# Optimization experiments

Measured on AMD Instinct MI355X. Metric: run time of the kernel, lower is better.

The kernel has to match this reference:

```python
import jax, jax.numpy as jnp
import numpy as np
from jax import lax
import math

B, L, D = 2, 1024, 1024
H = 16
HD = D // H
DS = 16            # d_state
EXP = 2
DIN = EXP * D      # d_inner = 2048
DCONV = 4
DTR = math.ceil(D / 16)  # dt_rank = 64
EPS = 1e-5


def setup_inputs() -> dict:
    key = jax.random.key(0)
    ks = jax.random.split(key, 24)
    g = lambda i, shape, s=0.02: (jax.random.normal(ks[i], shape, dtype=jnp.float32) * s)
    A_log = jnp.log(jnp.tile(jnp.arange(1, DS + 1, dtype=jnp.float32)[None, :], (DIN, 1)))
    return {
        "x": jax.random.normal(ks[0], (B, L, D), dtype=jnp.float32),
        # MambaWrapper pre-norm
        "mnorm_w": jnp.ones((D,), jnp.float32), "mnorm_b": jnp.zeros((D,), jnp.float32),
        # MambaBlock params
        "in_proj_w": g(1, (2 * DIN, D)),
        "conv_w": g(2, (DIN, 1, DCONV), 0.1), "conv_b": jnp.zeros((DIN,), jnp.float32),
        "x_proj_w": g(3, (DTR + 2 * DS, DIN)),
        "dt_proj_w": g(4, (DIN, DTR)), "dt_proj_b": g(5, (DIN,), 0.01),
        "A_log": A_log, "D_skip": jnp.ones((DIN,), jnp.float32),
        "out_proj_w": g(6, (D, DIN)),
        # attention branch
        "norm1_w": jnp.ones((D,), jnp.float32), "norm1_b": jnp.zeros((D,), jnp.float32),
        "wqkv_w": g(7, (D + 2 * HD, D)), "wqkv_b": jnp.zeros((D + 2 * HD,), jnp.float32),
        "oattn_w": g(8, (D, D)), "oattn_b": jnp.zeros((D,), jnp.float32),
        # parallel fusion: Linear(2D->D) + LayerNorm
        "fuse_w": g(9, (D, 2 * D)), "fuse_b": jnp.zeros((D,), jnp.float32),
        "fln_w": jnp.ones((D,), jnp.float32), "fln_b": jnp.zeros((D,), jnp.float32),
    }


def _ln(x, w, b):
    m = x.mean(-1, keepdims=True)
    xc = x - m
    v = (xc * xc).mean(-1, keepdims=True)
    return xc * lax.rsqrt(v + EPS) * w + b


def _selective_scan(u, delta, A, Bm, Cm, D_skip):
    # u, delta: (b,l,din); A: (din,n); Bm,Cm: (b,l,n)
    dA = jnp.exp(delta[..., None] * A)                    # (b,l,din,n)
    dBu = delta[..., None] * Bm[:, :, None, :] * u[..., None]

    def step(h, inp):
        dA_t, dBu_t, C_t = inp                            # (b,din,n),(b,din,n),(b,n)
        h = dA_t * h + dBu_t
        y = jnp.einsum('bdn,bn->bd', h, C_t)
        return h, y

    h0 = jnp.zeros((u.shape[0], u.shape[2], A.shape[1]), u.dtype)
    _, ys = lax.scan(step, h0, (dA.transpose(1, 0, 2, 3), dBu.transpose(1, 0, 2, 3), Cm.transpose(1, 0, 2)))
    return ys.transpose(1, 0, 2) + u * D_skip             # (b,l,din)


def _mamba_branch(x, mnorm_w, mnorm_b, in_proj_w, conv_w, conv_b, x_proj_w,
                  dt_proj_w, dt_proj_b, A_log, D_skip, out_proj_w):
    xn = _ln(x, mnorm_w, mnorm_b)
    xr = xn @ in_proj_w.T                                 # (b,l,2*din)
    u, res = xr[..., :DIN], xr[..., DIN:]
    # depthwise causal conv1d (torch pads d_conv-1 both sides then slices [:l])
    uc = u.transpose(0, 2, 1)                             # (b,din,l)
    uc = lax.conv_general_dilated(uc, conv_w, (1,), [(DCONV - 1, 0)],
                                  dimension_numbers=('NCH', 'OIH', 'NCH'),
                                  feature_group_count=DIN) + conv_b[None, :, None]
    u = jax.nn.silu(uc.transpose(0, 2, 1))
    dbc = u @ x_proj_w.T                                  # (b,l,dtr+2n)
    delta = jax.nn.softplus(dbc[..., :DTR] @ dt_proj_w.T + dt_proj_b)
    Bm = dbc[..., DTR:DTR + DS]
    Cm = dbc[..., DTR + DS:]
    y = _selective_scan(u, delta, -jnp.exp(A_log), Bm, Cm, D_skip)
    y = y * jax.nn.silu(res)
    return (y @ out_proj_w.T) + x                         # dropout=identity (eval), +residual


def _mqa_branch(x, norm1_w, norm1_b, wqkv_w, wqkv_b, oattn_w, oattn_b):
    xn = _ln(x, norm1_w, norm1_b)
    qkv = xn @ wqkv_w.T + wqkv_b
    q = qkv[..., :D].reshape(B, L, H, HD)
    k = qkv[..., D:D + HD]                                # shared single K head (b,l,hd)
    v = qkv[..., D + HD:]
    scores = jnp.einsum('blhd,bsd->bhls', q, k) / math.sqrt(HD)
    causal = jnp.tril(jnp.ones((L, L), bool))
    scores = jnp.where(causal, scores, jnp.finfo(scores.dtype).min)
    attn = jax.nn.softmax(scores, axis=-1)
    o = jnp.einsum('bhls,bsd->blhd', attn, v).reshape(B, L, D)
    return x + (o @ oattn_w.T + oattn_b)


def reference(x, mnorm_w, mnorm_b, in_proj_w, conv_w, conv_b, x_proj_w,
              dt_proj_w, dt_proj_b, A_log, D_skip, out_proj_w,
              norm1_w, norm1_b, wqkv_w, wqkv_b, oattn_w, oattn_b,
              fuse_w, fuse_b, fln_w, fln_b):
    mamba_out = _mamba_branch(x, mnorm_w, mnorm_b, in_proj_w, conv_w, conv_b, x_proj_w,
                              dt_proj_w, dt_proj_b, A_log, D_skip, out_proj_w)
    attn_out = _mqa_branch(x, norm1_w, norm1_b, wqkv_w, wqkv_b, oattn_w, oattn_b)
    combined = jnp.concatenate([mamba_out, attn_out], axis=-1)
    fused = _ln(combined @ fuse_w.T + fuse_b, fln_w, fln_b)
    return fused
```

## Files before the change

kernel.cpp:

```cpp
#include <hip/hip_runtime.h>
#include <hip/hip_bf16.h>
#include <hip/hip_fp16.h>
#include <cstddef>


using bf16 = __hip_bfloat16;
using frag8 = __attribute__((ext_vector_type(8))) short;
using f32x4 = __attribute__((ext_vector_type(4))) float;

__device__ __forceinline__ float siluf(float x) { return x / (1.f + __expf(-x)); }

__device__ __forceinline__ int sigmode(const unsigned int* sig) {
    const unsigned int s = *sig;
    return s == 0x3F800000u ? 1 : (s == 0x3C003C00u ? 2 : 0);
}
__device__ __forceinline__ float ldx(const void* p, size_t i, int m) {
    if (m == 1) return reinterpret_cast<const float*>(p)[i];
    if (m == 2) return __half2float(reinterpret_cast<const __half*>(p)[i]);
    return __bfloat162float(reinterpret_cast<const bf16*>(p)[i]);
}

__device__ __forceinline__ void gload_lds16(const void* g, void* l) {
    __builtin_amdgcn_global_load_lds(
        (const __attribute__((address_space(1))) unsigned int*)g,
        (__attribute__((address_space(3))) unsigned int*)l, 16, 0, 0);
}

__global__ void sentinel_kernel(float* out, float code) {
    if (threadIdx.x == 0) out[0] = code;
}

__global__ __launch_bounds__(256) void wconv_kernel(const void* __restrict__ W, size_t off,
                                                    bf16* __restrict__ dst, int total8,
                                                    const unsigned int* __restrict__ sig) {
    const int g = blockIdx.x * 256 + threadIdx.x;
    if (g >= total8) return;
    const int md = sigmode(sig);
    const size_t i0 = off + (size_t)g * 8;
    union { bf16 h[8]; uint4 v; } u;
    if (md == 0) {
        u.v = *reinterpret_cast<const uint4*>((const bf16*)W + i0);
    } else {
#pragma unroll
        for (int j = 0; j < 8; ++j) u.h[j] = __float2bfloat16(ldx(W, i0 + j, md));
    }
    *reinterpret_cast<uint4*>(dst + (size_t)g * 8) = u.v;
}

__global__ __launch_bounds__(256) void wconv2_kernel(
    const void* __restrict__ W1, bf16* __restrict__ dst1, int total8_1,
    const void* __restrict__ W2, bf16* __restrict__ dst2, int total8_2,
    const unsigned int* __restrict__ sig) {
    const int g = blockIdx.x * 256 + threadIdx.x;
    const int md = sigmode(sig);
    const void* W;
    bf16* dst;
    int gg;
    if (g < total8_1) { W = W1; dst = dst1; gg = g; }
    else if (g < total8_1 + total8_2) { W = W2; dst = dst2; gg = g - total8_1; }
    else return;
    const size_t i0 = (size_t)gg * 8;
    union { bf16 h[8]; uint4 v; } u;
    if (md == 0) {
        u.v = *reinterpret_cast<const uint4*>((const bf16*)W + i0);
    } else {
#pragma unroll
        for (int j = 0; j < 8; ++j) u.h[j] = __float2bfloat16(ldx(W, i0 + j, md));
    }
    *reinterpret_cast<uint4*>(dst + i0) = u.v;
}

template <typename TO>
__global__ __launch_bounds__(256) void ln_kernel(
    const void* __restrict__ x, int x_from_in,
    const void* __restrict__ w, const void* __restrict__ b,
    const unsigned int* __restrict__ sig, TO* __restrict__ out) {
    const int md = sigmode(sig);
    const int xm = x_from_in ? md : 0;
    const int row = blockIdx.x;
    const int tid = threadIdx.x;
    __shared__ float red[256];
    const size_t base = (size_t)row * 1024;
    float v[4];
    float s = 0.f;
#pragma unroll
    for (int i = 0; i < 4; ++i) { v[i] = ldx(x, base + tid + i * 256, xm); s += v[i]; }
    red[tid] = s;
    __syncthreads();
    for (int st = 128; st > 0; st >>= 1) {
        if (tid < st) red[tid] += red[tid + st];
        __syncthreads();
    }
    const float mean = red[0] * (1.f / 1024.f);
    __syncthreads();
    float s2 = 0.f;
#pragma unroll
    for (int i = 0; i < 4; ++i) { v[i] -= mean; s2 += v[i] * v[i]; }
    red[tid] = s2;
    __syncthreads();
    for (int st = 128; st > 0; st >>= 1) {
        if (tid < st) red[tid] += red[tid + st];
        __syncthreads();
    }
    const float inv = rsqrtf(red[0] * (1.f / 1024.f) + 1e-5f);
#pragma unroll
    for (int i = 0; i < 4; ++i) {
        const int d = tid + i * 256;
        const float r = v[i] * inv * ldx(w, d, md) + ldx(b, d, md);
        if constexpr (sizeof(TO) == 4) out[base + d] = r;
        else out[base + d] = __float2bfloat16(r);
    }
}

template <int BM>
__global__ __launch_bounds__(256) void mfma_gemm(
    const bf16* __restrict__ A1, const bf16* __restrict__ A2, int KA1, int lda,
    const bf16* __restrict__ Wb,
    const void* __restrict__ bias,
    const void* __restrict__ resid, int ldr,
    bf16* __restrict__ C, int ldc,
    int K, int Nbound, int act, const unsigned int* __restrict__ sig,
    bf16* __restrict__ vt) {
    constexpr int NFR = (BM == 128) ? 4 : 2;
    const int md = sigmode(sig);
    __shared__ __align__(16) bf16 Als[BM * 32];
    __shared__ __align__(16) bf16 Wls[128 * 32];
    const int tid = threadIdx.x;
    const int lane = tid & 63;
    const int w = tid >> 6;
    const int arow = (BM == 128) ? ((w >> 1) * 64) : 0;
    const int bcol = (BM == 128) ? ((w & 1) * 64) : (w * 32);
    const int m0 = blockIdx.y * BM;
    const int n0 = blockIdx.x * 128;
    f32x4 acc[4][NFR];
#pragma unroll
    for (int i = 0; i < 4; ++i)
#pragma unroll
        for (int j = 0; j < NFR; ++j) acc[i][j] = {0.f, 0.f, 0.f, 0.f};
    const int fm = lane & 15;
    const int fq = lane >> 4;
    for (int kk = 0; kk < K; kk += 32) {
        if constexpr (BM == 128) {
#pragma unroll
            for (int i = 0; i < 2; ++i) {
                const int chunk = i * 256 + tid;
                const int r = chunk >> 2, q = chunk & 3;
                const int gk = kk + q * 8;
                const bf16* srcA = (A2 != nullptr && gk >= KA1)
                    ? (A2 + (size_t)(m0 + r) * lda + (gk - KA1))
                    : (A1 + (size_t)(m0 + r) * lda + gk);
                gload_lds16(srcA, (char*)Als + (size_t)(i * 256 + w * 64) * 16);
            }
        } else {
            const int r = tid >> 2, q = tid & 3;
            const int gk = kk + q * 8;
            const bf16* srcA = (A2 != nullptr && gk >= KA1)
                ? (A2 + (size_t)(m0 + r) * lda + (gk - KA1))
                : (A1 + (size_t)(m0 + r) * lda + gk);
            gload_lds16(srcA, (char*)Als + (size_t)(w * 64) * 16);
        }
#pragma unroll
        for (int i = 0; i < 2; ++i) {
            const int chunk = i * 256 + tid;
            const int r = chunk >> 2, q = chunk & 3;
            const bf16* srcW = Wb + (size_t)(n0 + r) * K + kk + q * 8;
            gload_lds16(srcW, (char*)Wls + (size_t)(i * 256 + w * 64) * 16);
        }
        __syncthreads();
        frag8 af[4], bfr[NFR];
#pragma unroll
        for (int ms = 0; ms < 4; ++ms)
            af[ms] = *reinterpret_cast<const frag8*>(&Als[(size_t)(arow + ms * 16 + fm) * 32 + fq * 8]);
#pragma unroll
        for (int ns = 0; ns < NFR; ++ns)
            bfr[ns] = *reinterpret_cast<const frag8*>(&Wls[(size_t)(bcol + ns * 16 + fm) * 32 + fq * 8]);
#pragma unroll
        for (int ms = 0; ms < 4; ++ms)
#pragma unroll
            for (int ns = 0; ns < NFR; ++ns)
                acc[ms][ns] = __builtin_amdgcn_mfma_f32_16x16x32_bf16(af[ms], bfr[ns], acc[ms][ns], 0, 0, 0);
        __syncthreads();
    }
#pragma unroll
    for (int ms = 0; ms < 4; ++ms) {
#pragma unroll
        for (int r = 0; r < 4; ++r) {
            const int m = m0 + arow + ms * 16 + fq * 4 + r;
#pragma unroll
            for (int ns = 0; ns < NFR; ++ns) {
                const int n = n0 + bcol + ns * 16 + fm;
                if (n < Nbound) {
                    float v = acc[ms][ns][r];
                    if (bias) v += ldx(bias, n, md);
                    if (resid) v += ldx(resid, (size_t)m * ldr + n, md);
                    if (act == 1) v = (v > 20.f) ? v : log1pf(expf(v));
                    const bf16 hv = __float2bfloat16(v);
                    C[(size_t)m * ldc + n] = hv;
                    if (vt != nullptr && n >= 1088) {
                        vt[((size_t)((m >> 10) * 64 + (n - 1088))) * 1024 + (m & 1023)] = hv;
                    }
                }
            }
        }
    }
}

__global__ __launch_bounds__(256) void conv_silu_kernel(
    const bf16* __restrict__ u0, int us, const void* __restrict__ cw,
    const void* __restrict__ cb, const unsigned int* __restrict__ sig,
    bf16* __restrict__ u) {
    const int md = sigmode(sig);
    const int idx = blockIdx.x * 256 + threadIdx.x;
    const int c8 = (idx & 255) * 8;
    const int bl = idx >> 8;
    const int l = bl & 1023;
    float acc[8];
#pragma unroll
    for (int i = 0; i < 8; ++i) acc[i] = ldx(cb, c8 + i, md);
#pragma unroll
    for (int k = 0; k < 4; ++k) {
        const int ls = l - 3 + k;
        if (ls >= 0) {
            union { frag8 v; bf16 h[8]; } uin;
            uin.v = *reinterpret_cast<const frag8*>(u0 + (size_t)(bl - 3 + k) * us + c8);
#pragma unroll
            for (int i = 0; i < 8; ++i)
                acc[i] += __bfloat162float(uin.h[i]) * ldx(cw, (c8 + i) * 4 + k, md);
        }
    }
    union { frag8 v; bf16 h[8]; } uo;
#pragma unroll
    for (int i = 0; i < 8; ++i) uo.h[i] = __float2bfloat16(siluf(acc[i]));
    *reinterpret_cast<frag8*>(u + (size_t)bl * 2048 + c8) = uo.v;
}

__global__ __launch_bounds__(512) void scan_kernel(
    bf16* __restrict__ delta_y, const bf16* __restrict__ u,
    const bf16* __restrict__ dbc, const bf16* __restrict__ res,
    const void* __restrict__ A_log, const void* __restrict__ D_skip,
    const unsigned int* __restrict__ sig) {
    constexpr int DYS = 4096;
    constexpr int US  = 2048;
    constexpr int BS  = 96;
    constexpr int PRS = 20;
    constexpr int PJS = 168;
    const int md = sigmode(sig);
    const int n = threadIdx.x & 15;
    const int j = threadIdx.x >> 4;
    const int bx = blockIdx.x;
    const int c = ((bx & 7) << 8) | (bx >> 3);
    const int b = blockIdx.y;
    __shared__ float Ac[32 * 17], Hc[32 * 17], h0s[32 * 17];
    __shared__ __align__(16) float P[32 * PJS];
    __shared__ __align__(16) bf16 Dcol[1024], Ucol[1024];
    const float acoef = -expf(ldx(A_log, c * 16 + n, md));
    const float dsk = ldx(D_skip, c, md);
    const int t0 = j * 32;
    const int bt0 = b * 1024 + t0;

    {
        const int tid = threadIdx.x;
#pragma unroll
        for (int rr = 0; rr < 2; ++rr) {
            const int t = tid + rr * 512;
            Dcol[t] = delta_y[(size_t)(b * 1024 + t) * DYS + c];
            Ucol[t] = u[(size_t)(b * 1024 + t) * US + c];
        }
    }
    __syncthreads();

    {
        const bf16* pb = dbc + (size_t)bt0 * BS + 64 + n;
        float hloc = 0.f, aprod = 1.f;
#pragma unroll 8
        for (int tt = 0; tt < 32; ++tt) {
            const float dlt = __bfloat162float(Dcol[t0 + tt]);
            const float ut = __bfloat162float(Ucol[t0 + tt]);
            const float Bn = __bfloat162float(*pb);
            const float a = __expf(dlt * acoef);
            hloc = a * hloc + dlt * Bn * ut;
            aprod *= a;
            pb += BS;
        }
        Ac[j * 17 + n] = aprod;
        Hc[j * 17 + n] = hloc;
    }
    __syncthreads();
    if (threadIdx.x < 16) {
        float e = 0.f;
        for (int jj = 0; jj < 32; ++jj) {
            h0s[jj * 17 + threadIdx.x] = e;
            e = Ac[jj * 17 + threadIdx.x] * e + Hc[jj * 17 + threadIdx.x];
        }
    }
    __syncthreads();

    float h = h0s[j * 17 + n];
    float psum[2];
    float* Pj = &P[j * PJS];
    {
        const bf16* pb = dbc + (size_t)bt0 * BS + 64 + n;
        const int nq = n >> 3;
        const int nr = n & 7;
#pragma unroll
        for (int q = 0; q < 4; ++q) {
#pragma unroll
            for (int k = 0; k < 8; ++k) {
                const int tt = q * 8 + k;
                const float dlt = __bfloat162float(Dcol[t0 + tt]);
                const float ut = __bfloat162float(Ucol[t0 + tt]);
                const float Bn = __bfloat162float(pb[0]);
                const float Cn = __bfloat162float(pb[16]);
                const float a = __expf(dlt * acoef);
                h = a * h + dlt * Bn * ut;
                Pj[k * PRS + n] = h * Cn;
                pb += BS;
            }
            if (nq == (q & 1)) {
                const f32x4* pr = reinterpret_cast<const f32x4*>(&Pj[nr * PRS]);
                float s = 0.f;
#pragma unroll
                for (int v = 0; v < 4; ++v) {
                    const f32x4 q4 = pr[v];
                    s += q4[0] + q4[1] + q4[2] + q4[3];
                }
                psum[q >> 1] = s;
            }
        }
    }
#pragma unroll
    for (int half = 0; half < 2; ++half) {
        const int tl = t0 + half * 16 + n;
        const size_t id = (size_t)(b * 1024 + tl) * DYS + c;
        const float ut = __bfloat162float(Ucol[tl]);
        const float r = __bfloat162float(res[id]);
        delta_y[id] = __float2bfloat16((psum[half] + ut * dsk) * siluf(r));
    }
}

__global__ __launch_bounds__(128) void attn_mfma(const bf16* __restrict__ qkv,
                                                 const bf16* __restrict__ Vt,
                                                 bf16* __restrict__ o) {
    const int tid = threadIdx.x;
    const int lane = tid & 63;
    const int wv = tid >> 6;
    const int fm = lane & 15, quad = lane >> 4;
    const int qt = blockIdx.x, h = blockIdx.y, b = blockIdx.z;
    __shared__ __align__(16) bf16 Pls[2][64][72];
    __shared__ float Ols[64][68];
    __shared__ float Mst[64], Lst[64];

    frag8 qf[4][2];
#pragma unroll
    for (int ms = 0; ms < 4; ++ms)
#pragma unroll
        for (int kq = 0; kq < 2; ++kq)
            qf[ms][kq] = *reinterpret_cast<const frag8*>(
                qkv + ((size_t)(b * 1024 + qt * 64 + ms * 16 + fm)) * 1152 + h * 64 + kq * 32 + quad * 8);

    float mrun[4][4], lrun[4][4];
    f32x4 acco[4][4];
#pragma unroll
    for (int ms = 0; ms < 4; ++ms)
#pragma unroll
        for (int r = 0; r < 4; ++r) { mrun[ms][r] = -1.0e30f; lrun[ms][r] = 0.f; }
#pragma unroll
    for (int ms = 0; ms < 4; ++ms)
#pragma unroll
        for (int nd = 0; nd < 4; ++nd) acco[ms][nd] = {0.f, 0.f, 0.f, 0.f};

    for (int st = wv; st <= qt; st += 2) {
        f32x4 accs[4][4];
#pragma unroll
        for (int ms = 0; ms < 4; ++ms)
#pragma unroll
            for (int ns = 0; ns < 4; ++ns) accs[ms][ns] = {0.f, 0.f, 0.f, 0.f};
        __builtin_amdgcn_s_setprio(1);
#pragma unroll
        for (int ns = 0; ns < 4; ++ns) {
            frag8 kf[2];
#pragma unroll
            for (int kq = 0; kq < 2; ++kq)
                kf[kq] = *reinterpret_cast<const frag8*>(
                    qkv + ((size_t)(b * 1024 + st * 64 + ns * 16 + fm)) * 1152 + 1024 + kq * 32 + quad * 8);
#pragma unroll
            for (int ms = 0; ms < 4; ++ms) {
                accs[ms][ns] = __builtin_amdgcn_mfma_f32_16x16x32_bf16(qf[ms][0], kf[0], accs[ms][ns], 0, 0, 0);
                accs[ms][ns] = __builtin_amdgcn_mfma_f32_16x16x32_bf16(qf[ms][1], kf[1], accs[ms][ns], 0, 0, 0);
            }
        }
        __builtin_amdgcn_s_setprio(0);
        const bool diag = (st == qt);
#pragma unroll
        for (int ms = 0; ms < 4; ++ms) {
            float alpha[4];
#pragma unroll
            for (int r = 0; r < 4; ++r) {
                const int ql = ms * 16 + quad * 4 + r;
                float sv[4];
#pragma unroll
                for (int ns = 0; ns < 4; ++ns) {
                    const int sl = ns * 16 + fm;
                    sv[ns] = (!diag || sl <= ql) ? accs[ms][ns][r] * 0.125f : -1.0e30f;
                }
                float mloc = fmaxf(fmaxf(sv[0], sv[1]), fmaxf(sv[2], sv[3]));
                mloc = fmaxf(mloc, __shfl_xor(mloc, 1));
                mloc = fmaxf(mloc, __shfl_xor(mloc, 2));
                mloc = fmaxf(mloc, __shfl_xor(mloc, 4));
                mloc = fmaxf(mloc, __shfl_xor(mloc, 8));
                const float mnew = fmaxf(mrun[ms][r], mloc);
                alpha[r] = __expf(mrun[ms][r] - mnew);
                float rs = 0.f;
#pragma unroll
                for (int ns = 0; ns < 4; ++ns) {
                    const float p = __expf(sv[ns] - mnew);
                    rs += p;
                    Pls[wv][ms * 16 + quad * 4 + r][ns * 16 + fm] = __float2bfloat16(p);
                }
                rs += __shfl_xor(rs, 1);
                rs += __shfl_xor(rs, 2);
                rs += __shfl_xor(rs, 4);
                rs += __shfl_xor(rs, 8);
                lrun[ms][r] = lrun[ms][r] * alpha[r] + rs;
                mrun[ms][r] = mnew;
            }
#pragma unroll
            for (int nd = 0; nd < 4; ++nd)
#pragma unroll
                for (int r = 0; r < 4; ++r) acco[ms][nd][r] *= alpha[r];
        }
        frag8 pf[4][2];
#pragma unroll
        for (int ms = 0; ms < 4; ++ms)
#pragma unroll
            for (int ks = 0; ks < 2; ++ks)
                pf[ms][ks] = *reinterpret_cast<const frag8*>(&Pls[wv][ms * 16 + fm][ks * 32 + quad * 8]);
        __builtin_amdgcn_s_setprio(1);
#pragma unroll
        for (int nd = 0; nd < 4; ++nd) {
            frag8 vf[2];
#pragma unroll
            for (int ks = 0; ks < 2; ++ks)
                vf[ks] = *reinterpret_cast<const frag8*>(
                    Vt + ((size_t)b * 64 + nd * 16 + fm) * 1024 + st * 64 + ks * 32 + quad * 8);
#pragma unroll
            for (int ms = 0; ms < 4; ++ms) {
                acco[ms][nd] = __builtin_amdgcn_mfma_f32_16x16x32_bf16(pf[ms][0], vf[0], acco[ms][nd], 0, 0, 0);
                acco[ms][nd] = __builtin_amdgcn_mfma_f32_16x16x32_bf16(pf[ms][1], vf[1], acco[ms][nd], 0, 0, 0);
            }
        }
        __builtin_amdgcn_s_setprio(0);
    }

    __syncthreads();
    if (wv == 1) {
#pragma unroll
        for (int ms = 0; ms < 4; ++ms)
#pragma unroll
            for (int r = 0; r < 4; ++r) {
                const int q = ms * 16 + quad * 4 + r;
                Mst[q] = mrun[ms][r];
                Lst[q] = lrun[ms][r];
#pragma unroll
                for (int nd = 0; nd < 4; ++nd)
                    Ols[q][nd * 16 + fm] = acco[ms][nd][r];
            }
    }
    __syncthreads();
    if (wv == 0) {
#pragma unroll
        for (int ms = 0; ms < 4; ++ms)
#pragma unroll
            for (int r = 0; r < 4; ++r) {
                const int q = ms * 16 + quad * 4 + r;
                const float m1 = Mst[q], l1 = Lst[q];
                const float M = fmaxf(mrun[ms][r], m1);
                const float a0 = __expf(mrun[ms][r] - M);
                const float a1 = __expf(m1 - M);
                const float L = lrun[ms][r] * a0 + l1 * a1;
                const float inv = 1.f / fmaxf(L, 1e-30f);
                const size_t row = (size_t)(b * 1024 + qt * 64 + q);
#pragma unroll
                for (int nd = 0; nd < 4; ++nd)
                    o[row * 1024 + h * 64 + nd * 16 + fm] =
                        __float2bfloat16((acco[ms][nd][r] * a0 + Ols[q][nd * 16 + fm] * a1) * inv);
            }
    }
}

extern "C" void kernel_launch(void* const* d_in, const int* in_sizes, int n_in,
                              void* d_out, int out_size, void* d_ws, size_t ws_size,
                              hipStream_t stream) {
    float* out = (float*)d_out;

    static const int kExp[22] = {
        2097152, 1024, 1024, 4194304, 8192, 2048, 196608, 131072, 2048, 32768,
        2048, 2097152, 1024, 1024, 1179648, 1152, 1048576, 1024, 2097152, 1024,
        1024, 1024};
    const size_t kNeedBytes = 29360128;
    float code = 0.f;
    if (n_in != 22) code = 65536.f * (32 + (n_in & 31));
    else if (out_size != 2097152) code = 65536.f * 200.f;
    else {
        for (int i = 0; i < 22; ++i)
            if (in_sizes[i] != kExp[i]) { code = 65536.f * (64 + i); break; }
        if (code == 0.f && ws_size < kNeedBytes)
            code = 65536.f * (128.f + (float)(ws_size >> 20));
    }
    if (code != 0.f) {
        sentinel_kernel<<<dim3(1), dim3(64), 0, stream>>>(out, code);
        return;
    }

    const unsigned int* sig = (const unsigned int*)d_in[1];

    bf16* ws = (bf16*)d_ws;
    bf16* Aslot = ws;
    bf16* Bslot = ws + 2097152;
    bf16* Cslot = ws + 6291456;
    bf16* Dslot = ws + 10485760;
    bf16* dbc    = Aslot;
    bf16* xprojW = Aslot + 262144;
    bf16* dtW    = Aslot + 524288;
    bf16* u0res  = Bslot;
    bf16* mambaOut = Dslot;
    bf16* DsHi = Dslot + 2097152;
    bf16* BsHi = Bslot + 2097152;
    bf16* Vt   = Bslot + 1572864;

    const dim3 b256(256);
    const int NOSPLIT = 1 << 30;
    const int NB = 1 << 30;

    ln_kernel<bf16><<<dim3(2048), b256, 0, stream>>>(d_in[0], 1, d_in[1], d_in[2], sig, Aslot);
    wconv_kernel<<<dim3(2048), b256, 0, stream>>>(d_in[3], 0, Dslot, 524288, sig);
    mfma_gemm<128><<<dim3(32, 16), b256, 0, stream>>>(Aslot, nullptr, NOSPLIT, 1024,
        Dslot, nullptr, nullptr, 0, u0res, 4096, 1024, NB, 0, sig, nullptr);
    conv_silu_kernel<<<dim3(2048), b256, 0, stream>>>(u0res, 4096, d_in[4], d_in[5], sig, Dslot);
    wconv2_kernel<<<dim3(160), b256, 0, stream>>>(d_in[6], xprojW, 24576, d_in[7], dtW, 16384, sig);
    mfma_gemm<128><<<dim3(1, 16), b256, 0, stream>>>(Dslot, nullptr, NOSPLIT, 2048,
        xprojW, nullptr, nullptr, 0, dbc, 96, 2048, 96, 0, sig, nullptr);
    mfma_gemm<128><<<dim3(16, 16), b256, 0, stream>>>(dbc, nullptr, NOSPLIT, 96,
        dtW, d_in[8], nullptr, 0, u0res, 4096, 64, NB, 1, sig, nullptr);
    scan_kernel<<<dim3(2048, 2), dim3(512), 0, stream>>>(u0res, Dslot, dbc, u0res + 2048,
        d_in[9], d_in[10], sig);
    wconv_kernel<<<dim3(1024), b256, 0, stream>>>(d_in[11], 0, DsHi, 262144, sig);
    mfma_gemm<64><<<dim3(8, 32), b256, 0, stream>>>(u0res, nullptr, NOSPLIT, 4096,
        DsHi, nullptr, d_in[0], 1024, mambaOut, 1024, 2048, NB, 0, sig, nullptr);

    ln_kernel<bf16><<<dim3(2048), b256, 0, stream>>>(d_in[0], 1, d_in[12], d_in[13], sig, Aslot);
    wconv_kernel<<<dim3(576), b256, 0, stream>>>(d_in[14], 0, Bslot, 147456, sig);
    mfma_gemm<64><<<dim3(9, 32), b256, 0, stream>>>(Aslot, nullptr, NOSPLIT, 1024,
        Bslot, d_in[15], nullptr, 0, Cslot, 1152, 1024, NB, 0, sig, Vt);
    attn_mfma<<<dim3(16, 16, 2), dim3(128), 0, stream>>>(Cslot, Vt, DsHi);
    wconv_kernel<<<dim3(512), b256, 0, stream>>>(d_in[16], 0, Bslot, 131072, sig);
    mfma_gemm<64><<<dim3(8, 32), b256, 0, stream>>>(DsHi, nullptr, NOSPLIT, 1024,
        Bslot, d_in[17], d_in[0], 1024, BsHi, 1024, 1024, NB, 0, sig, nullptr);

    wconv_kernel<<<dim3(1024), b256, 0, stream>>>(d_in[18], 0, Cslot, 262144, sig);
    mfma_gemm<64><<<dim3(8, 32), b256, 0, stream>>>(mambaOut, BsHi, 1024, 1024,
        Cslot, d_in[19], nullptr, 0, Aslot, 1024, 2048, NB, 0, sig, nullptr);
    ln_kernel<float><<<dim3(2048), b256, 0, stream>>>(Aslot, 0, d_in[20], d_in[21], sig, out);
}
```

Baseline: 673.8 us.

## Add narrow-N GEMM tiles and cache dBu in registers in scan

Adds a BN template parameter to the MFMA GEMM so the N=1024 and N=1152 GEMMs run with 64-wide column tiles. This doubles the block count to fill more CUs, and the dt_proj GEMM moves to BM=64. In the selective scan, the first pass keeps each timestep's dt*B*u in a register array and batches the strided B and C loads, so the second pass no longer reloads B and u. The costs are lower per-block reuse in the GEMMs and more registers in the scan kernel.

After: 623.0 us. 1.08x faster.

```diff
diff --git a/kernel.cpp b/kernel.cpp
--- a/kernel.cpp
+++ b/kernel.cpp
@@ -112,7 +112,7 @@
     }
 }
 
-template <int BM>
+template <int BM, int BN>
 __global__ __launch_bounds__(256) void mfma_gemm(
     const bf16* __restrict__ A1, const bf16* __restrict__ A2, int KA1, int lda,
     const bf16* __restrict__ Wb,
@@ -121,17 +121,17 @@
     bf16* __restrict__ C, int ldc,
     int K, int Nbound, int act, const unsigned int* __restrict__ sig,
     bf16* __restrict__ vt) {
-    constexpr int NFR = (BM == 128) ? 4 : 2;
+    constexpr int NFR = (BN == 64) ? 1 : ((BM == 128) ? 4 : 2);
     const int md = sigmode(sig);
     __shared__ __align__(16) bf16 Als[BM * 32];
-    __shared__ __align__(16) bf16 Wls[128 * 32];
+    __shared__ __align__(16) bf16 Wls[BN * 32];
     const int tid = threadIdx.x;
     const int lane = tid & 63;
     const int w = tid >> 6;
     const int arow = (BM == 128) ? ((w >> 1) * 64) : 0;
-    const int bcol = (BM == 128) ? ((w & 1) * 64) : (w * 32);
+    const int bcol = (BN == 64) ? (w * 16) : ((BM == 128) ? ((w & 1) * 64) : (w * 32));
     const int m0 = blockIdx.y * BM;
-    const int n0 = blockIdx.x * 128;
+    const int n0 = blockIdx.x * BN;
     f32x4 acc[4][NFR];
 #pragma unroll
     for (int i = 0; i < 4; ++i)
@@ -160,7 +160,7 @@
             gload_lds16(srcA, (char*)Als + (size_t)(w * 64) * 16);
         }
 #pragma unroll
-        for (int i = 0; i < 2; ++i) {
+        for (int i = 0; i < (BN == 64 ? 1 : 2); ++i) {
             const int chunk = i * 256 + tid;
             const int r = chunk >> 2, q = chunk & 3;
             const bf16* srcW = Wb + (size_t)(n0 + r) * K + kk + q * 8;
@@ -269,18 +269,28 @@
     }
     __syncthreads();
 
+    float dv[32];
+
     {
         const bf16* pb = dbc + (size_t)bt0 * BS + 64 + n;
         float hloc = 0.f, aprod = 1.f;
-#pragma unroll 8
-        for (int tt = 0; tt < 32; ++tt) {
-            const float dlt = __bfloat162float(Dcol[t0 + tt]);
-            const float ut = __bfloat162float(Ucol[t0 + tt]);
-            const float Bn = __bfloat162float(*pb);
-            const float a = __expf(dlt * acoef);
-            hloc = a * hloc + dlt * Bn * ut;
-            aprod *= a;
-            pb += BS;
+#pragma unroll
+        for (int g = 0; g < 2; ++g) {
+            bf16 Bv[16];
+#pragma unroll
+            for (int k = 0; k < 16; ++k) Bv[k] = pb[(size_t)(g * 16 + k) * BS];
+#pragma unroll
+            for (int k = 0; k < 16; ++k) {
+                const int tt = g * 16 + k;
+                const float dlt = __bfloat162float(Dcol[t0 + tt]);
+                const float ut = __bfloat162float(Ucol[t0 + tt]);
+                const float Bn = __bfloat162float(Bv[k]);
+                const float a = __expf(dlt * acoef);
+                const float dBu = dlt * Bn * ut;
+                dv[tt] = dBu;
+                hloc = a * hloc + dBu;
+                aprod *= a;
+            }
         }
         Ac[j * 17 + n] = aprod;
         Hc[j * 17 + n] = hloc;
@@ -299,22 +309,21 @@
     float psum[2];
     float* Pj = &P[j * PJS];
     {
-        const bf16* pb = dbc + (size_t)bt0 * BS + 64 + n;
+        const bf16* pc = dbc + (size_t)bt0 * BS + 80 + n;
         const int nq = n >> 3;
         const int nr = n & 7;
 #pragma unroll
         for (int q = 0; q < 4; ++q) {
+            bf16 Cv[8];
+#pragma unroll
+            for (int k = 0; k < 8; ++k) Cv[k] = pc[(size_t)(q * 8 + k) * BS];
 #pragma unroll
             for (int k = 0; k < 8; ++k) {
                 const int tt = q * 8 + k;
                 const float dlt = __bfloat162float(Dcol[t0 + tt]);
-                const float ut = __bfloat162float(Ucol[t0 + tt]);
-                const float Bn = __bfloat162float(pb[0]);
-                const float Cn = __bfloat162float(pb[16]);
                 const float a = __expf(dlt * acoef);
-                h = a * h + dlt * Bn * ut;
-                Pj[k * PRS + n] = h * Cn;
-                pb += BS;
+                h = a * h + dv[tt];
+                Pj[k * PRS + n] = h * __bfloat162float(Cv[k]);
             }
             if (nq == (q & 1)) {
                 const f32x4* pr = reinterpret_cast<const f32x4*>(&Pj[nr * PRS]);
@@ -534,31 +543,31 @@
 
     ln_kernel<bf16><<<dim3(2048), b256, 0, stream>>>(d_in[0], 1, d_in[1], d_in[2], sig, Aslot);
     wconv_kernel<<<dim3(2048), b256, 0, stream>>>(d_in[3], 0, Dslot, 524288, sig);
-    mfma_gemm<128><<<dim3(32, 16), b256, 0, stream>>>(Aslot, nullptr, NOSPLIT, 1024,
+    mfma_gemm<128, 128><<<dim3(32, 16), b256, 0, stream>>>(Aslot, nullptr, NOSPLIT, 1024,
         Dslot, nullptr, nullptr, 0, u0res, 4096, 1024, NB, 0, sig, nullptr);
     conv_silu_kernel<<<dim3(2048), b256, 0, stream>>>(u0res, 4096, d_in[4], d_in[5], sig, Dslot);
     wconv2_kernel<<<dim3(160), b256, 0, stream>>>(d_in[6], xprojW, 24576, d_in[7], dtW, 16384, sig);
-    mfma_gemm<128><<<dim3(1, 16), b256, 0, stream>>>(Dslot, nullptr, NOSPLIT, 2048,
+    mfma_gemm<128, 128><<<dim3(1, 16), b256, 0, stream>>>(Dslot, nullptr, NOSPLIT, 2048,
         xprojW, nullptr, nullptr, 0, dbc, 96, 2048, 96, 0, sig, nullptr);
-    mfma_gemm<128><<<dim3(16, 16), b256, 0, stream>>>(dbc, nullptr, NOSPLIT, 96,
+    mfma_gemm<64, 128><<<dim3(16, 32), b256, 0, stream>>>(dbc, nullptr, NOSPLIT, 96,
         dtW, d_in[8], nullptr, 0, u0res, 4096, 64, NB, 1, sig, nullptr);
     scan_kernel<<<dim3(2048, 2), dim3(512), 0, stream>>>(u0res, Dslot, dbc, u0res + 2048,
         d_in[9], d_in[10], sig);
     wconv_kernel<<<dim3(1024), b256, 0, stream>>>(d_in[11], 0, DsHi, 262144, sig);
-    mfma_gemm<64><<<dim3(8, 32), b256, 0, stream>>>(u0res, nullptr, NOSPLIT, 4096,
+    mfma_gemm<64, 64><<<dim3(16, 32), b256, 0, stream>>>(u0res, nullptr, NOSPLIT, 4096,
         DsHi, nullptr, d_in[0], 1024, mambaOut, 1024, 2048, NB, 0, sig, nullptr);
 
     ln_kernel<bf16><<<dim3(2048), b256, 0, stream>>>(d_in[0], 1, d_in[12], d_in[13], sig, Aslot);
     wconv_kernel<<<dim3(576), b256, 0, stream>>>(d_in[14], 0, Bslot, 147456, sig);
-    mfma_gemm<64><<<dim3(9, 32), b256, 0, stream>>>(Aslot, nullptr, NOSPLIT, 1024,
+    mfma_gemm<64, 64><<<dim3(18, 32), b256, 0, stream>>>(Aslot, nullptr, NOSPLIT, 1024,
         Bslot, d_in[15], nullptr, 0, Cslot, 1152, 1024, NB, 0, sig, Vt);
     attn_mfma<<<dim3(16, 16, 2), dim3(128), 0, stream>>>(Cslot, Vt, DsHi);
     wconv_kernel<<<dim3(512), b256, 0, stream>>>(d_in[16], 0, Bslot, 131072, sig);
-    mfma_gemm<64><<<dim3(8, 32), b256, 0, stream>>>(DsHi, nullptr, NOSPLIT, 1024,
+    mfma_gemm<64, 64><<<dim3(16, 32), b256, 0, stream>>>(DsHi, nullptr, NOSPLIT, 1024,
         Bslot, d_in[17], d_in[0], 1024, BsHi, 1024, 1024, NB, 0, sig, nullptr);
 
     wconv_kernel<<<dim3(1024), b256, 0, stream>>>(d_in[18], 0, Cslot, 262144, sig);
-    mfma_gemm<64><<<dim3(8, 32), b256, 0, stream>>>(mambaOut, BsHi, 1024, 1024,
+    mfma_gemm<64, 64><<<dim3(16, 32), b256, 0, stream>>>(mambaOut, BsHi, 1024, 1024,
         Cslot, d_in[19], nullptr, 0, Aslot, 1024, 2048, NB, 0, sig, nullptr);
     ln_kernel<float><<<dim3(2048), b256, 0, stream>>>(Aslot, 0, d_in[20], d_in[21], sig, out);
 }
```
